# Kernel optimization log

Measured on AMD Instinct MI355X. Metric: run time of the kernel, lower is better.

## Reference

```python
import jax, jax.numpy as jnp
import numpy as np

EPS = 1e-12  # torch.nn.functional.normalize default eps


def _l2norm(x, axis):
    n = jnp.sqrt(jnp.sum(x * x, axis=axis, keepdims=True))
    return x / jnp.maximum(n, EPS)


def setup_inputs() -> dict:
    key = jax.random.key(0)
    k1, k2 = jax.random.split(key)
    B, n_with_neg, neighbor, n_facet, emb_dim = 4096, 1, 128, 8, 16
    features = jax.random.normal(k1, (B, n_with_neg, n_facet * emb_dim), dtype=jnp.float32)
    metapath_features = jax.random.normal(
        k2, (B, n_with_neg, neighbor, n_facet * emb_dim), dtype=jnp.float32)
    return {
        "features": features,
        "metapath_features": metapath_features,
        "emb_dim": emb_dim,
        "n_facet": n_facet,
        "n_iter": 4,
    }


def reference(features, metapath_features, emb_dim, n_facet, n_iter):
    B, n = features.shape[0], features.shape[1]
    N = metapath_features.shape[2]
    # x: [B, n, F, D], z: [B, n, N, F, D]
    x = features.reshape(B, n, n_facet, emb_dim)
    z = metapath_features.reshape(B, n, N, n_facet, emb_dim)
    x = _l2norm(x, axis=3)
    z = _l2norm(z, axis=4)
    u = x
    for clus_iter in range(n_iter):
        # routing logits: dot over emb_dim -> [B, n, N, F]
        p = jnp.einsum('bnkfd,bnfd->bnkf', z, u)
        p = jax.nn.softmax(p, axis=3)
        # weighted sum over neighbors -> [B, n, F, D]
        u = jnp.einsum('bnkfd,bnkf->bnfd', z, p) + x
        if clus_iter < n_iter - 1:
            u = _l2norm(u, axis=3)
    return u.reshape(B, n_facet * emb_dim)
```

## Files before the change

kernel.cpp:

```cpp
#include <hip/hip_runtime.h>
#include <math.h>


#define CC 128
#define LOG2E 1.44269504088896340736f

typedef float f32x2 __attribute__((ext_vector_type(2)));
typedef unsigned u32x2 __attribute__((ext_vector_type(2)));

template<int CTRL>
__device__ __forceinline__ float dpp_add(float x) {
    int y = __builtin_amdgcn_update_dpp(0, __float_as_int(x), CTRL, 0xF, 0xF, true);
    return x + __int_as_float(y);
}
#define DPP_XOR1 0xB1
#define DPP_XOR2 0x4E
#define DPP_HMIR 0x141
#define DPP_MIR  0x140

__device__ __forceinline__ f32x2 xor16_add2(f32x2 v) {
    u32x2 r0 = __builtin_amdgcn_permlane16_swap(__float_as_uint(v.x), __float_as_uint(v.x), false, false);
    u32x2 r1 = __builtin_amdgcn_permlane16_swap(__float_as_uint(v.y), __float_as_uint(v.y), false, false);
    f32x2 o;
    o.x = __uint_as_float(r0.x) + __uint_as_float(r0.y);
    o.y = __uint_as_float(r1.x) + __uint_as_float(r1.y);
    return o;
}
__device__ __forceinline__ f32x2 xor32_add2(f32x2 v) {
    u32x2 r0 = __builtin_amdgcn_permlane32_swap(__float_as_uint(v.x), __float_as_uint(v.x), false, false);
    u32x2 r1 = __builtin_amdgcn_permlane32_swap(__float_as_uint(v.y), __float_as_uint(v.y), false, false);
    f32x2 o;
    o.x = __uint_as_float(r0.x) + __uint_as_float(r0.y);
    o.y = __uint_as_float(r1.x) + __uint_as_float(r1.y);
    return o;
}
__device__ __forceinline__ float rsq_guard(float s) {
    return __builtin_amdgcn_rsqf(fmaxf(s, 1e-24f));
}
__device__ __forceinline__ unsigned pack_bf16(float lo, float hi) {
    unsigned r;
    asm("v_cvt_pk_bf16_f32 %0, %1, %2" : "=v"(r) : "v"(lo), "v"(hi));
    return r;
}
__device__ __forceinline__ f32x2 unpack_bf16(unsigned u) {
    f32x2 r;
    r.x = __uint_as_float(u << 16);
    r.y = __uint_as_float(u & 0xFFFF0000u);
    return r;
}

__global__ __launch_bounds__(512, 8)
void hete_routing_kernel(const float* __restrict__ feat,
                         const float* __restrict__ mp,
                         float* __restrict__ out)
{
    __shared__ float part[8][CC];
    __shared__ float u_s[CC];

    const int t = threadIdx.x;
    const int wave = t >> 6;
    const int lane = t & 63;
    const int cg = lane & 15;
    const int kgl = lane >> 4;
    const int kq = wave * 4 + kgl;
    const int c0 = cg * 8;
    const int b = blockIdx.x;

    unsigned zp[4][4];
    {
        const float* zb = mp + (size_t)b * (128 * CC) + kq * 4 * CC + c0;
        float4 A[4], Bv[4];
#pragma unroll
        for (int kk = 0; kk < 4; ++kk) {
            A[kk]  = *reinterpret_cast<const float4*>(zb + kk * CC);
            Bv[kk] = *reinterpret_cast<const float4*>(zb + kk * CC + 4);
        }
#pragma unroll
        for (int kk = 0; kk < 4; ++kk) {
            float s = A[kk].x * A[kk].x + A[kk].y * A[kk].y
                    + A[kk].z * A[kk].z + A[kk].w * A[kk].w
                    + Bv[kk].x * Bv[kk].x + Bv[kk].y * Bv[kk].y
                    + Bv[kk].z * Bv[kk].z + Bv[kk].w * Bv[kk].w;
            s = dpp_add<DPP_XOR1>(s);
            const float inv = rsq_guard(s);
            zp[kk][0] = pack_bf16(A[kk].x * inv,  A[kk].y * inv);
            zp[kk][1] = pack_bf16(A[kk].z * inv,  A[kk].w * inv);
            zp[kk][2] = pack_bf16(Bv[kk].x * inv, Bv[kk].y * inv);
            zp[kk][3] = pack_bf16(Bv[kk].z * inv, Bv[kk].w * inv);
        }
    }

    float xh = 0.f;
    if (t < CC) {
        const float xv = feat[(size_t)b * CC + t];
        float s = xv * xv;
        s = dpp_add<DPP_XOR1>(s);
        s = dpp_add<DPP_XOR2>(s);
        s = dpp_add<DPP_HMIR>(s);
        s = dpp_add<DPP_MIR>(s);
        xh = xv * rsq_guard(s);
        u_s[t] = xh * LOG2E;
    }
    __syncthreads();

#pragma unroll
    for (int it = 0; it < 4; ++it) {
        f32x2 ur[4];
        {
            const float4 A  = *reinterpret_cast<const float4*>(&u_s[c0]);
            const float4 Bv = *reinterpret_cast<const float4*>(&u_s[c0 + 4]);
            ur[0] = f32x2{A.x, A.y};  ur[1] = f32x2{A.z, A.w};
            ur[2] = f32x2{Bv.x, Bv.y}; ur[3] = f32x2{Bv.z, Bv.w};
        }

        f32x2 pu[4] = {f32x2{0.f,0.f}, f32x2{0.f,0.f}, f32x2{0.f,0.f}, f32x2{0.f,0.f}};
#pragma unroll
        for (int kk = 0; kk < 4; ++kk) {
            const f32x2 z0 = unpack_bf16(zp[kk][0]);
            const f32x2 z1 = unpack_bf16(zp[kk][1]);
            const f32x2 z2 = unpack_bf16(zp[kk][2]);
            const f32x2 z3 = unpack_bf16(zp[kk][3]);
            f32x2 acc = z0 * ur[0];
            acc += z1 * ur[1];
            acc += z2 * ur[2];
            acc += z3 * ur[3];
            const float l = dpp_add<DPP_XOR1>(acc.x + acc.y);
            const float e = __builtin_amdgcn_exp2f(l);
            float su = dpp_add<DPP_XOR2>(e);
            su = dpp_add<DPP_HMIR>(su);
            su = dpp_add<DPP_MIR>(su);
            const float wk = e * __builtin_amdgcn_rcpf(su);
            const f32x2 ws = {wk, wk};
            pu[0] += z0 * ws;
            pu[1] += z1 * ws;
            pu[2] += z2 * ws;
            pu[3] += z3 * ws;
        }
#pragma unroll
        for (int j = 0; j < 4; ++j) {
            pu[j] = xor16_add2(pu[j]);
            pu[j] = xor32_add2(pu[j]);
        }
        if (kgl == 0) {
            float* dst = &part[wave][c0];
            *reinterpret_cast<float4*>(dst)     = make_float4(pu[0].x, pu[0].y, pu[1].x, pu[1].y);
            *reinterpret_cast<float4*>(dst + 4) = make_float4(pu[2].x, pu[2].y, pu[3].x, pu[3].y);
        }
        __syncthreads();

        if (t < CC) {
            float un = xh;
#pragma unroll
            for (int j = 0; j < 8; ++j) un += part[j][t];
            if (it < 3) {
                float s = un * un;
                s = dpp_add<DPP_XOR1>(s);
                s = dpp_add<DPP_XOR2>(s);
                s = dpp_add<DPP_HMIR>(s);
                s = dpp_add<DPP_MIR>(s);
                u_s[t] = un * rsq_guard(s) * LOG2E;
            } else {
                out[(size_t)b * CC + t] = un;
            }
        }
        if (it < 3) __syncthreads();
    }
}

extern "C" void kernel_launch(void* const* d_in, const int* in_sizes, int n_in,
                              void* d_out, int out_size, void* d_ws, size_t ws_size,
                              hipStream_t stream) {
    const float* feat = (const float*)d_in[0];
    const float* mp   = (const float*)d_in[1];
    float* out = (float*)d_out;
    const int B = in_sizes[0] / CC;
    hete_routing_kernel<<<B, 512, 0, stream>>>(feat, mp, out);
}
```

Measured before the change: 48.11 us.

## Process four batches per block with register prefetch of the next batch

Each block now handles four consecutive batch rows instead of one. It prefetches the next row's neighbor features and input features into registers during the first routing iteration of the current row, overlapping global loads with compute. The grid shrinks fourfold and the launch-bounds occupancy hint drops from 8 to 5 blocks per CU to leave room for the extra live prefetch registers. The trade-off is fewer resident waves available to hide memory latency, and the grid size now assumes the batch divides evenly by four.

```diff
diff --git a/kernel.cpp b/kernel.cpp
--- a/kernel.cpp
+++ b/kernel.cpp
@@ -3,6 +3,8 @@
 
 
 #define CC 128
+#define NB 4
+#define ZSZ (128 * CC)
 #define LOG2E 1.44269504088896340736f
 
 typedef float f32x2 __attribute__((ext_vector_type(2)));
@@ -49,7 +51,7 @@
     return r;
 }
 
-__global__ __launch_bounds__(512, 8)
+__global__ __launch_bounds__(512, 5)
 void hete_routing_kernel(const float* __restrict__ feat,
                          const float* __restrict__ mp,
                          float* __restrict__ out)
@@ -64,17 +66,22 @@
     const int kgl = lane >> 4;
     const int kq = wave * 4 + kgl;
     const int c0 = cg * 8;
-    const int b = blockIdx.x;
+    const int b0 = blockIdx.x * NB;
 
-    unsigned zp[4][4];
-    {
-        const float* zb = mp + (size_t)b * (128 * CC) + kq * 4 * CC + c0;
-        float4 A[4], Bv[4];
+    const float* zb = mp + (size_t)b0 * ZSZ + kq * 4 * CC + c0;
+
+    float4 A[4], Bv[4];
 #pragma unroll
-        for (int kk = 0; kk < 4; ++kk) {
-            A[kk]  = *reinterpret_cast<const float4*>(zb + kk * CC);
-            Bv[kk] = *reinterpret_cast<const float4*>(zb + kk * CC + 4);
-        }
+    for (int kk = 0; kk < 4; ++kk) {
+        A[kk]  = *reinterpret_cast<const float4*>(zb + kk * CC);
+        Bv[kk] = *reinterpret_cast<const float4*>(zb + kk * CC + 4);
+    }
+    float xv = 0.f;
+    if (t < CC) xv = feat[(size_t)b0 * CC + t];
+
+#pragma unroll 1
+    for (int i = 0; i < NB; ++i) {
+        unsigned zp[4][4];
 #pragma unroll
         for (int kk = 0; kk < 4; ++kk) {
             float s = A[kk].x * A[kk].x + A[kk].y * A[kk].y
@@ -88,82 +95,91 @@
             zp[kk][2] = pack_bf16(Bv[kk].x * inv, Bv[kk].y * inv);
             zp[kk][3] = pack_bf16(Bv[kk].z * inv, Bv[kk].w * inv);
         }
-    }
 
-    float xh = 0.f;
-    if (t < CC) {
-        const float xv = feat[(size_t)b * CC + t];
-        float s = xv * xv;
-        s = dpp_add<DPP_XOR1>(s);
-        s = dpp_add<DPP_XOR2>(s);
-        s = dpp_add<DPP_HMIR>(s);
-        s = dpp_add<DPP_MIR>(s);
-        xh = xv * rsq_guard(s);
-        u_s[t] = xh * LOG2E;
-    }
-    __syncthreads();
-
-#pragma unroll
-    for (int it = 0; it < 4; ++it) {
-        f32x2 ur[4];
-        {
-            const float4 A  = *reinterpret_cast<const float4*>(&u_s[c0]);
-            const float4 Bv = *reinterpret_cast<const float4*>(&u_s[c0 + 4]);
-            ur[0] = f32x2{A.x, A.y};  ur[1] = f32x2{A.z, A.w};
-            ur[2] = f32x2{Bv.x, Bv.y}; ur[3] = f32x2{Bv.z, Bv.w};
-        }
-
-        f32x2 pu[4] = {f32x2{0.f,0.f}, f32x2{0.f,0.f}, f32x2{0.f,0.f}, f32x2{0.f,0.f}};
-#pragma unroll
-        for (int kk = 0; kk < 4; ++kk) {
-            const f32x2 z0 = unpack_bf16(zp[kk][0]);
-            const f32x2 z1 = unpack_bf16(zp[kk][1]);
-            const f32x2 z2 = unpack_bf16(zp[kk][2]);
-            const f32x2 z3 = unpack_bf16(zp[kk][3]);
-            f32x2 acc = z0 * ur[0];
-            acc += z1 * ur[1];
-            acc += z2 * ur[2];
-            acc += z3 * ur[3];
-            const float l = dpp_add<DPP_XOR1>(acc.x + acc.y);
-            const float e = __builtin_amdgcn_exp2f(l);
-            float su = dpp_add<DPP_XOR2>(e);
-            su = dpp_add<DPP_HMIR>(su);
-            su = dpp_add<DPP_MIR>(su);
-            const float wk = e * __builtin_amdgcn_rcpf(su);
-            const f32x2 ws = {wk, wk};
-            pu[0] += z0 * ws;
-            pu[1] += z1 * ws;
-            pu[2] += z2 * ws;
-            pu[3] += z3 * ws;
-        }
-#pragma unroll
-        for (int j = 0; j < 4; ++j) {
-            pu[j] = xor16_add2(pu[j]);
-            pu[j] = xor32_add2(pu[j]);
-        }
-        if (kgl == 0) {
-            float* dst = &part[wave][c0];
-            *reinterpret_cast<float4*>(dst)     = make_float4(pu[0].x, pu[0].y, pu[1].x, pu[1].y);
-            *reinterpret_cast<float4*>(dst + 4) = make_float4(pu[2].x, pu[2].y, pu[3].x, pu[3].y);
+        float xh = 0.f;
+        if (t < CC) {
+            float s = xv * xv;
+            s = dpp_add<DPP_XOR1>(s);
+            s = dpp_add<DPP_XOR2>(s);
+            s = dpp_add<DPP_HMIR>(s);
+            s = dpp_add<DPP_MIR>(s);
+            xh = xv * rsq_guard(s);
+            u_s[t] = xh * LOG2E;
         }
         __syncthreads();
 
-        if (t < CC) {
-            float un = xh;
 #pragma unroll
-            for (int j = 0; j < 8; ++j) un += part[j][t];
-            if (it < 3) {
-                float s = un * un;
-                s = dpp_add<DPP_XOR1>(s);
-                s = dpp_add<DPP_XOR2>(s);
-                s = dpp_add<DPP_HMIR>(s);
-                s = dpp_add<DPP_MIR>(s);
-                u_s[t] = un * rsq_guard(s) * LOG2E;
-            } else {
-                out[(size_t)b * CC + t] = un;
+        for (int it = 0; it < 4; ++it) {
+            if (it == 0 && i + 1 < NB) {
+                const float* zn = zb + (size_t)(i + 1) * ZSZ;
+#pragma unroll
+                for (int kk = 0; kk < 4; ++kk) {
+                    A[kk]  = *reinterpret_cast<const float4*>(zn + kk * CC);
+                    Bv[kk] = *reinterpret_cast<const float4*>(zn + kk * CC + 4);
+                }
+                if (t < CC) xv = feat[(size_t)(b0 + i + 1) * CC + t];
             }
+
+            f32x2 ur[4];
+            {
+                const float4 Ua = *reinterpret_cast<const float4*>(&u_s[c0]);
+                const float4 Ub = *reinterpret_cast<const float4*>(&u_s[c0 + 4]);
+                ur[0] = f32x2{Ua.x, Ua.y};  ur[1] = f32x2{Ua.z, Ua.w};
+                ur[2] = f32x2{Ub.x, Ub.y};  ur[3] = f32x2{Ub.z, Ub.w};
+            }
+
+            f32x2 pu[4] = {f32x2{0.f,0.f}, f32x2{0.f,0.f}, f32x2{0.f,0.f}, f32x2{0.f,0.f}};
+#pragma unroll
+            for (int kk = 0; kk < 4; ++kk) {
+                const f32x2 z0 = unpack_bf16(zp[kk][0]);
+                const f32x2 z1 = unpack_bf16(zp[kk][1]);
+                const f32x2 z2 = unpack_bf16(zp[kk][2]);
+                const f32x2 z3 = unpack_bf16(zp[kk][3]);
+                f32x2 acc = z0 * ur[0];
+                acc += z1 * ur[1];
+                acc += z2 * ur[2];
+                acc += z3 * ur[3];
+                const float l = dpp_add<DPP_XOR1>(acc.x + acc.y);
+                const float e = __builtin_amdgcn_exp2f(l);
+                float su = dpp_add<DPP_XOR2>(e);
+                su = dpp_add<DPP_HMIR>(su);
+                su = dpp_add<DPP_MIR>(su);
+                const float wk = e * __builtin_amdgcn_rcpf(su);
+                const f32x2 ws = {wk, wk};
+                pu[0] += z0 * ws;
+                pu[1] += z1 * ws;
+                pu[2] += z2 * ws;
+                pu[3] += z3 * ws;
+            }
+#pragma unroll
+            for (int j = 0; j < 4; ++j) {
+                pu[j] = xor16_add2(pu[j]);
+                pu[j] = xor32_add2(pu[j]);
+            }
+            if (kgl == 0) {
+                float* dst = &part[wave][c0];
+                *reinterpret_cast<float4*>(dst)     = make_float4(pu[0].x, pu[0].y, pu[1].x, pu[1].y);
+                *reinterpret_cast<float4*>(dst + 4) = make_float4(pu[2].x, pu[2].y, pu[3].x, pu[3].y);
+            }
+            __syncthreads();
+
+            if (t < CC) {
+                float un = xh;
+#pragma unroll
+                for (int j = 0; j < 8; ++j) un += part[j][t];
+                if (it < 3) {
+                    float s = un * un;
+                    s = dpp_add<DPP_XOR1>(s);
+                    s = dpp_add<DPP_XOR2>(s);
+                    s = dpp_add<DPP_HMIR>(s);
+                    s = dpp_add<DPP_MIR>(s);
+                    u_s[t] = un * rsq_guard(s) * LOG2E;
+                } else {
+                    out[(size_t)(b0 + i) * CC + t] = un;
+                }
+            }
+            if (it < 3) __syncthreads();
         }
-        if (it < 3) __syncthreads();
     }
 }
 
@@ -174,5 +190,5 @@
     const float* mp   = (const float*)d_in[1];
     float* out = (float*)d_out;
     const int B = in_sizes[0] / CC;
-    hete_routing_kernel<<<B, 512, 0, stream>>>(feat, mp, out);
+    hete_routing_kernel<<<B / NB, 512, 0, stream>>>(feat, mp, out);
 }
```

Measured after the change: 61.24 us. 27.3% more time.

## Remap threads so each lane holds 4 channels across 8 neighbors with coalesced loads

Applied to the files above, without the earlier changes.

Changes the work mapping so each wave loads 16 contiguous neighbor rows as float4 per lane, with 32 lanes covering one 128-channel row. Neighbors are now unrolled 8 per lane instead of 4, and each lane holds 4 channels instead of 8. The facet dot product needs two DPP steps, the softmax sum over facets uses a half-mirror, a mirror and a permlane16 swap, and the neighbor reduction needs only one permlane32 step. This is meant to make global loads fully contiguous and to cut the cross-lane reduction work at the end of each iteration. The cost is more per-neighbor softmax reductions and exp/rcp calls per lane.

```diff
diff --git a/kernel.cpp b/kernel.cpp
--- a/kernel.cpp
+++ b/kernel.cpp
@@ -18,13 +18,9 @@
 #define DPP_HMIR 0x141
 #define DPP_MIR  0x140
 
-__device__ __forceinline__ f32x2 xor16_add2(f32x2 v) {
-    u32x2 r0 = __builtin_amdgcn_permlane16_swap(__float_as_uint(v.x), __float_as_uint(v.x), false, false);
-    u32x2 r1 = __builtin_amdgcn_permlane16_swap(__float_as_uint(v.y), __float_as_uint(v.y), false, false);
-    f32x2 o;
-    o.x = __uint_as_float(r0.x) + __uint_as_float(r0.y);
-    o.y = __uint_as_float(r1.x) + __uint_as_float(r1.y);
-    return o;
+__device__ __forceinline__ float xor16_add(float v) {
+    u32x2 r = __builtin_amdgcn_permlane16_swap(__float_as_uint(v), __float_as_uint(v), false, false);
+    return __uint_as_float(r.x) + __uint_as_float(r.y);
 }
 __device__ __forceinline__ f32x2 xor32_add2(f32x2 v) {
     u32x2 r0 = __builtin_amdgcn_permlane32_swap(__float_as_uint(v.x), __float_as_uint(v.x), false, false);
@@ -58,37 +54,16 @@
     __shared__ float u_s[CC];
 
     const int t = threadIdx.x;
-    const int wave = t >> 6;
-    const int lane = t & 63;
-    const int cg = lane & 15;
-    const int kgl = lane >> 4;
-    const int kq = wave * 4 + kgl;
-    const int c0 = cg * 8;
+    const int w = t >> 6;
+    const int l = t & 63;
+    const int q = l & 31;
     const int b = blockIdx.x;
 
-    unsigned zp[4][4];
-    {
-        const float* zb = mp + (size_t)b * (128 * CC) + kq * 4 * CC + c0;
-        float4 A[4], Bv[4];
+    const float* zg = mp + (size_t)b * (128 * CC) + w * 2048 + l * 4;
+    float4 raw[8];
 #pragma unroll
-        for (int kk = 0; kk < 4; ++kk) {
-            A[kk]  = *reinterpret_cast<const float4*>(zb + kk * CC);
-            Bv[kk] = *reinterpret_cast<const float4*>(zb + kk * CC + 4);
-        }
-#pragma unroll
-        for (int kk = 0; kk < 4; ++kk) {
-            float s = A[kk].x * A[kk].x + A[kk].y * A[kk].y
-                    + A[kk].z * A[kk].z + A[kk].w * A[kk].w
-                    + Bv[kk].x * Bv[kk].x + Bv[kk].y * Bv[kk].y
-                    + Bv[kk].z * Bv[kk].z + Bv[kk].w * Bv[kk].w;
-            s = dpp_add<DPP_XOR1>(s);
-            const float inv = rsq_guard(s);
-            zp[kk][0] = pack_bf16(A[kk].x * inv,  A[kk].y * inv);
-            zp[kk][1] = pack_bf16(A[kk].z * inv,  A[kk].w * inv);
-            zp[kk][2] = pack_bf16(Bv[kk].x * inv, Bv[kk].y * inv);
-            zp[kk][3] = pack_bf16(Bv[kk].z * inv, Bv[kk].w * inv);
-        }
-    }
+    for (int j = 0; j < 8; ++j)
+        raw[j] = *reinterpret_cast<const float4*>(zg + j * 256);
 
     float xh = 0.f;
     if (t < CC) {
@@ -101,50 +76,53 @@
         xh = xv * rsq_guard(s);
         u_s[t] = xh * LOG2E;
     }
+
+    unsigned zp[8][2];
+#pragma unroll
+    for (int j = 0; j < 8; ++j) {
+        float s = raw[j].x * raw[j].x + raw[j].y * raw[j].y
+                + raw[j].z * raw[j].z + raw[j].w * raw[j].w;
+        s = dpp_add<DPP_XOR1>(s);
+        s = dpp_add<DPP_XOR2>(s);
+        const float inv = rsq_guard(s);
+        zp[j][0] = pack_bf16(raw[j].x * inv, raw[j].y * inv);
+        zp[j][1] = pack_bf16(raw[j].z * inv, raw[j].w * inv);
+    }
     __syncthreads();
 
 #pragma unroll
     for (int it = 0; it < 4; ++it) {
-        f32x2 ur[4];
+        f32x2 ur0, ur1;
         {
-            const float4 A  = *reinterpret_cast<const float4*>(&u_s[c0]);
-            const float4 Bv = *reinterpret_cast<const float4*>(&u_s[c0 + 4]);
-            ur[0] = f32x2{A.x, A.y};  ur[1] = f32x2{A.z, A.w};
-            ur[2] = f32x2{Bv.x, Bv.y}; ur[3] = f32x2{Bv.z, Bv.w};
+            const float4 U = *reinterpret_cast<const float4*>(&u_s[q * 4]);
+            ur0 = f32x2{U.x, U.y};
+            ur1 = f32x2{U.z, U.w};
         }
 
-        f32x2 pu[4] = {f32x2{0.f,0.f}, f32x2{0.f,0.f}, f32x2{0.f,0.f}, f32x2{0.f,0.f}};
+        f32x2 pu0 = {0.f, 0.f}, pu1 = {0.f, 0.f};
 #pragma unroll
-        for (int kk = 0; kk < 4; ++kk) {
-            const f32x2 z0 = unpack_bf16(zp[kk][0]);
-            const f32x2 z1 = unpack_bf16(zp[kk][1]);
-            const f32x2 z2 = unpack_bf16(zp[kk][2]);
-            const f32x2 z3 = unpack_bf16(zp[kk][3]);
-            f32x2 acc = z0 * ur[0];
-            acc += z1 * ur[1];
-            acc += z2 * ur[2];
-            acc += z3 * ur[3];
-            const float l = dpp_add<DPP_XOR1>(acc.x + acc.y);
-            const float e = __builtin_amdgcn_exp2f(l);
-            float su = dpp_add<DPP_XOR2>(e);
-            su = dpp_add<DPP_HMIR>(su);
+        for (int j = 0; j < 8; ++j) {
+            const f32x2 z0 = unpack_bf16(zp[j][0]);
+            const f32x2 z1 = unpack_bf16(zp[j][1]);
+            f32x2 acc = z0 * ur0;
+            acc += z1 * ur1;
+            float d = acc.x + acc.y;
+            d = dpp_add<DPP_XOR1>(d);
+            d = dpp_add<DPP_XOR2>(d);
+            const float e = __builtin_amdgcn_exp2f(d);
+            float su = dpp_add<DPP_HMIR>(e);
             su = dpp_add<DPP_MIR>(su);
+            su = xor16_add(su);
             const float wk = e * __builtin_amdgcn_rcpf(su);
             const f32x2 ws = {wk, wk};
-            pu[0] += z0 * ws;
-            pu[1] += z1 * ws;
-            pu[2] += z2 * ws;
-            pu[3] += z3 * ws;
+            pu0 += z0 * ws;
+            pu1 += z1 * ws;
         }
-#pragma unroll
-        for (int j = 0; j < 4; ++j) {
-            pu[j] = xor16_add2(pu[j]);
-            pu[j] = xor32_add2(pu[j]);
-        }
-        if (kgl == 0) {
-            float* dst = &part[wave][c0];
-            *reinterpret_cast<float4*>(dst)     = make_float4(pu[0].x, pu[0].y, pu[1].x, pu[1].y);
-            *reinterpret_cast<float4*>(dst + 4) = make_float4(pu[2].x, pu[2].y, pu[3].x, pu[3].y);
+        pu0 = xor32_add2(pu0);
+        pu1 = xor32_add2(pu1);
+        if (l < 32) {
+            *reinterpret_cast<float4*>(&part[w][q * 4]) =
+                make_float4(pu0.x, pu0.y, pu1.x, pu1.y);
         }
         __syncthreads();
 
```

Result: slower. 52.61 us (+9.3%).

## Process two batch rows per block to amortize barriers and launch overhead

Applied to the files above, without the earlier changes.

Each 512-thread block now handles two batch elements, keeping both sets of normalized bf16 neighbor vectors in registers and interleaving their routing iterations so the same barriers serve both. This halves the grid size and the number of per-iteration synchronizations per element, and gives each wave independent work to hide latency. In exchange, register use roughly doubles (launch bounds lowered to 6 waves/EU hint) and occupancy drops, and an odd B would leave the last row unprocessed.

```diff
diff --git a/kernel.cpp b/kernel.cpp
--- a/kernel.cpp
+++ b/kernel.cpp
@@ -3,6 +3,7 @@
 
 
 #define CC 128
+#define ZSZ (128 * CC)
 #define LOG2E 1.44269504088896340736f
 
 typedef float f32x2 __attribute__((ext_vector_type(2)));
@@ -49,13 +50,15 @@
     return r;
 }
 
-__global__ __launch_bounds__(512, 8)
+__global__ __launch_bounds__(512, 6)
 void hete_routing_kernel(const float* __restrict__ feat,
                          const float* __restrict__ mp,
                          float* __restrict__ out)
 {
-    __shared__ float part[8][CC];
-    __shared__ float u_s[CC];
+    __shared__ float part1[8][CC];
+    __shared__ float part2[8][CC];
+    __shared__ float u1_s[CC];
+    __shared__ float u2_s[CC];
 
     const int t = threadIdx.x;
     const int wave = t >> 6;
@@ -64,16 +67,17 @@
     const int kgl = lane >> 4;
     const int kq = wave * 4 + kgl;
     const int c0 = cg * 8;
-    const int b = blockIdx.x;
-
-    unsigned zp[4][4];
+    const int b1 = blockIdx.x * 2;
+    const int b2 = b1 + 1;
+
+    unsigned zp1[4][4], zp2[4][4];
     {
-        const float* zb = mp + (size_t)b * (128 * CC) + kq * 4 * CC + c0;
         float4 A[4], Bv[4];
-#pragma unroll
-        for (int kk = 0; kk < 4; ++kk) {
-            A[kk]  = *reinterpret_cast<const float4*>(zb + kk * CC);
-            Bv[kk] = *reinterpret_cast<const float4*>(zb + kk * CC + 4);
+        const float* z1 = mp + (size_t)b1 * ZSZ + kq * 4 * CC + c0;
+#pragma unroll
+        for (int kk = 0; kk < 4; ++kk) {
+            A[kk]  = *reinterpret_cast<const float4*>(z1 + kk * CC);
+            Bv[kk] = *reinterpret_cast<const float4*>(z1 + kk * CC + 4);
         }
 #pragma unroll
         for (int kk = 0; kk < 4; ++kk) {
@@ -83,84 +87,150 @@
                     + Bv[kk].z * Bv[kk].z + Bv[kk].w * Bv[kk].w;
             s = dpp_add<DPP_XOR1>(s);
             const float inv = rsq_guard(s);
-            zp[kk][0] = pack_bf16(A[kk].x * inv,  A[kk].y * inv);
-            zp[kk][1] = pack_bf16(A[kk].z * inv,  A[kk].w * inv);
-            zp[kk][2] = pack_bf16(Bv[kk].x * inv, Bv[kk].y * inv);
-            zp[kk][3] = pack_bf16(Bv[kk].z * inv, Bv[kk].w * inv);
+            zp1[kk][0] = pack_bf16(A[kk].x * inv,  A[kk].y * inv);
+            zp1[kk][1] = pack_bf16(A[kk].z * inv,  A[kk].w * inv);
+            zp1[kk][2] = pack_bf16(Bv[kk].x * inv, Bv[kk].y * inv);
+            zp1[kk][3] = pack_bf16(Bv[kk].z * inv, Bv[kk].w * inv);
+        }
+        const float* z2 = mp + (size_t)b2 * ZSZ + kq * 4 * CC + c0;
+#pragma unroll
+        for (int kk = 0; kk < 4; ++kk) {
+            A[kk]  = *reinterpret_cast<const float4*>(z2 + kk * CC);
+            Bv[kk] = *reinterpret_cast<const float4*>(z2 + kk * CC + 4);
+        }
+#pragma unroll
+        for (int kk = 0; kk < 4; ++kk) {
+            float s = A[kk].x * A[kk].x + A[kk].y * A[kk].y
+                    + A[kk].z * A[kk].z + A[kk].w * A[kk].w
+                    + Bv[kk].x * Bv[kk].x + Bv[kk].y * Bv[kk].y
+                    + Bv[kk].z * Bv[kk].z + Bv[kk].w * Bv[kk].w;
+            s = dpp_add<DPP_XOR1>(s);
+            const float inv = rsq_guard(s);
+            zp2[kk][0] = pack_bf16(A[kk].x * inv,  A[kk].y * inv);
+            zp2[kk][1] = pack_bf16(A[kk].z * inv,  A[kk].w * inv);
+            zp2[kk][2] = pack_bf16(Bv[kk].x * inv, Bv[kk].y * inv);
+            zp2[kk][3] = pack_bf16(Bv[kk].z * inv, Bv[kk].w * inv);
         }
     }
 
     float xh = 0.f;
-    if (t < CC) {
-        const float xv = feat[(size_t)b * CC + t];
+    if (t < 256) {
+        const int ch = t & 127;
+        const int bb = (t < CC) ? b1 : b2;
+        const float xv = feat[(size_t)bb * CC + ch];
         float s = xv * xv;
         s = dpp_add<DPP_XOR1>(s);
         s = dpp_add<DPP_XOR2>(s);
         s = dpp_add<DPP_HMIR>(s);
         s = dpp_add<DPP_MIR>(s);
         xh = xv * rsq_guard(s);
-        u_s[t] = xh * LOG2E;
+        if (t < CC) u1_s[ch] = xh * LOG2E;
+        else        u2_s[ch] = xh * LOG2E;
     }
     __syncthreads();
 
 #pragma unroll
     for (int it = 0; it < 4; ++it) {
-        f32x2 ur[4];
         {
-            const float4 A  = *reinterpret_cast<const float4*>(&u_s[c0]);
-            const float4 Bv = *reinterpret_cast<const float4*>(&u_s[c0 + 4]);
-            ur[0] = f32x2{A.x, A.y};  ur[1] = f32x2{A.z, A.w};
-            ur[2] = f32x2{Bv.x, Bv.y}; ur[3] = f32x2{Bv.z, Bv.w};
-        }
-
-        f32x2 pu[4] = {f32x2{0.f,0.f}, f32x2{0.f,0.f}, f32x2{0.f,0.f}, f32x2{0.f,0.f}};
-#pragma unroll
-        for (int kk = 0; kk < 4; ++kk) {
-            const f32x2 z0 = unpack_bf16(zp[kk][0]);
-            const f32x2 z1 = unpack_bf16(zp[kk][1]);
-            const f32x2 z2 = unpack_bf16(zp[kk][2]);
-            const f32x2 z3 = unpack_bf16(zp[kk][3]);
-            f32x2 acc = z0 * ur[0];
-            acc += z1 * ur[1];
-            acc += z2 * ur[2];
-            acc += z3 * ur[3];
-            const float l = dpp_add<DPP_XOR1>(acc.x + acc.y);
-            const float e = __builtin_amdgcn_exp2f(l);
-            float su = dpp_add<DPP_XOR2>(e);
-            su = dpp_add<DPP_HMIR>(su);
-            su = dpp_add<DPP_MIR>(su);
-            const float wk = e * __builtin_amdgcn_rcpf(su);
-            const f32x2 ws = {wk, wk};
-            pu[0] += z0 * ws;
-            pu[1] += z1 * ws;
-            pu[2] += z2 * ws;
-            pu[3] += z3 * ws;
-        }
-#pragma unroll
-        for (int j = 0; j < 4; ++j) {
-            pu[j] = xor16_add2(pu[j]);
-            pu[j] = xor32_add2(pu[j]);
-        }
-        if (kgl == 0) {
-            float* dst = &part[wave][c0];
-            *reinterpret_cast<float4*>(dst)     = make_float4(pu[0].x, pu[0].y, pu[1].x, pu[1].y);
-            *reinterpret_cast<float4*>(dst + 4) = make_float4(pu[2].x, pu[2].y, pu[3].x, pu[3].y);
+            f32x2 ur[4];
+            const float4 Ua = *reinterpret_cast<const float4*>(&u1_s[c0]);
+            const float4 Ub = *reinterpret_cast<const float4*>(&u1_s[c0 + 4]);
+            ur[0] = f32x2{Ua.x, Ua.y};  ur[1] = f32x2{Ua.z, Ua.w};
+            ur[2] = f32x2{Ub.x, Ub.y};  ur[3] = f32x2{Ub.z, Ub.w};
+            f32x2 pu[4] = {f32x2{0.f,0.f}, f32x2{0.f,0.f}, f32x2{0.f,0.f}, f32x2{0.f,0.f}};
+#pragma unroll
+            for (int kk = 0; kk < 4; ++kk) {
+                const f32x2 z0 = unpack_bf16(zp1[kk][0]);
+                const f32x2 z1 = unpack_bf16(zp1[kk][1]);
+                const f32x2 z2 = unpack_bf16(zp1[kk][2]);
+                const f32x2 z3 = unpack_bf16(zp1[kk][3]);
+                f32x2 acc = z0 * ur[0];
+                acc += z1 * ur[1];
+                acc += z2 * ur[2];
+                acc += z3 * ur[3];
+                const float l = dpp_add<DPP_XOR1>(acc.x + acc.y);
+                const float e = __builtin_amdgcn_exp2f(l);
+                float su = dpp_add<DPP_XOR2>(e);
+                su = dpp_add<DPP_HMIR>(su);
+                su = dpp_add<DPP_MIR>(su);
+                const float wk = e * __builtin_amdgcn_rcpf(su);
+                const f32x2 ws = {wk, wk};
+                pu[0] += z0 * ws;
+                pu[1] += z1 * ws;
+                pu[2] += z2 * ws;
+                pu[3] += z3 * ws;
+            }
+#pragma unroll
+            for (int j = 0; j < 4; ++j) {
+                pu[j] = xor16_add2(pu[j]);
+                pu[j] = xor32_add2(pu[j]);
+            }
+            if (kgl == 0) {
+                float* dst = &part1[wave][c0];
+                *reinterpret_cast<float4*>(dst)     = make_float4(pu[0].x, pu[0].y, pu[1].x, pu[1].y);
+                *reinterpret_cast<float4*>(dst + 4) = make_float4(pu[2].x, pu[2].y, pu[3].x, pu[3].y);
+            }
+        }
+        {
+            f32x2 ur[4];
+            const float4 Ua = *reinterpret_cast<const float4*>(&u2_s[c0]);
+            const float4 Ub = *reinterpret_cast<const float4*>(&u2_s[c0 + 4]);
+            ur[0] = f32x2{Ua.x, Ua.y};  ur[1] = f32x2{Ua.z, Ua.w};
+            ur[2] = f32x2{Ub.x, Ub.y};  ur[3] = f32x2{Ub.z, Ub.w};
+            f32x2 pu[4] = {f32x2{0.f,0.f}, f32x2{0.f,0.f}, f32x2{0.f,0.f}, f32x2{0.f,0.f}};
+#pragma unroll
+            for (int kk = 0; kk < 4; ++kk) {
+                const f32x2 z0 = unpack_bf16(zp2[kk][0]);
+                const f32x2 z1 = unpack_bf16(zp2[kk][1]);
+                const f32x2 z2 = unpack_bf16(zp2[kk][2]);
+                const f32x2 z3 = unpack_bf16(zp2[kk][3]);
+                f32x2 acc = z0 * ur[0];
+                acc += z1 * ur[1];
+                acc += z2 * ur[2];
+                acc += z3 * ur[3];
+                const float l = dpp_add<DPP_XOR1>(acc.x + acc.y);
+                const float e = __builtin_amdgcn_exp2f(l);
+                float su = dpp_add<DPP_XOR2>(e);
+                su = dpp_add<DPP_HMIR>(su);
+                su = dpp_add<DPP_MIR>(su);
+                const float wk = e * __builtin_amdgcn_rcpf(su);
+                const f32x2 ws = {wk, wk};
+                pu[0] += z0 * ws;
+                pu[1] += z1 * ws;
+                pu[2] += z2 * ws;
+                pu[3] += z3 * ws;
+            }
+#pragma unroll
+            for (int j = 0; j < 4; ++j) {
+                pu[j] = xor16_add2(pu[j]);
+                pu[j] = xor32_add2(pu[j]);
+            }
+            if (kgl == 0) {
+                float* dst = &part2[wave][c0];
+                *reinterpret_cast<float4*>(dst)     = make_float4(pu[0].x, pu[0].y, pu[1].x, pu[1].y);
+                *reinterpret_cast<float4*>(dst + 4) = make_float4(pu[2].x, pu[2].y, pu[3].x, pu[3].y);
+            }
         }
         __syncthreads();
 
-        if (t < CC) {
+        if (t < 256) {
+            const int ch = t & 127;
+            const float (*pp)[CC] = (t < CC) ? part1 : part2;
             float un = xh;
 #pragma unroll
-            for (int j = 0; j < 8; ++j) un += part[j][t];
+            for (int j = 0; j < 8; ++j) un += pp[j][ch];
             if (it < 3) {
                 float s = un * un;
                 s = dpp_add<DPP_XOR1>(s);
                 s = dpp_add<DPP_XOR2>(s);
                 s = dpp_add<DPP_HMIR>(s);
                 s = dpp_add<DPP_MIR>(s);
-                u_s[t] = un * rsq_guard(s) * LOG2E;
+                const float uo = un * rsq_guard(s) * LOG2E;
+                if (t < CC) u1_s[ch] = uo;
+                else        u2_s[ch] = uo;
             } else {
-                out[(size_t)b * CC + t] = un;
+                const int bb = (t < CC) ? b1 : b2;
+                out[(size_t)bb * CC + ch] = un;
             }
         }
         if (it < 3) __syncthreads();
@@ -174,5 +244,5 @@
     const float* mp   = (const float*)d_in[1];
     float* out = (float*)d_out;
     const int B = in_sizes[0] / CC;
-    hete_routing_kernel<<<B, 512, 0, stream>>>(feat, mp, out);
-}
+    hete_routing_kernel<<<B / 2, 512, 0, stream>>>(feat, mp, out);
+}
```

New measurement: 85.25 us. 1.77x slower.
